# Kernel optimization log

Hardware: AMD Instinct MI355X
Metric: run time of the kernel (lower is better)

Reference implementation:

```python
import jax, jax.numpy as jnp
import numpy as np

WIRES = 4
NUM_LAYERS = 2


def setup_inputs() -> dict:
    key = jax.random.key(0)
    k1, k2 = jax.random.split(key)
    x = jax.random.uniform(k1, (8192, 1, 28, 28), dtype=jnp.float32)
    params = jax.random.normal(k2, (NUM_LAYERS, WIRES), dtype=jnp.float32)
    return {"x": x, "params": params}


def _apply_ry(state, theta, wire):
    # state: (B, P, 2,2,2,2) real (RY/CNOT circuit keeps amplitudes real)
    s = jnp.moveaxis(state, 2 + wire, -1)
    a, b = s[..., 0], s[..., 1]
    theta = jnp.asarray(theta)
    theta = theta.reshape(theta.shape + (1,) * (a.ndim - theta.ndim))
    c, sn = jnp.cos(theta / 2), jnp.sin(theta / 2)
    s = jnp.stack([c * a - sn * b, sn * a + c * b], axis=-1)
    return jnp.moveaxis(s, -1, 2 + wire)


def _cnot(state, ctrl, tgt):
    s = jnp.moveaxis(state, (2 + ctrl, 2 + tgt), (-2, -1))
    s = jnp.stack([s[..., 0, :], s[..., 1, ::-1]], axis=-2)
    return jnp.moveaxis(s, (-2, -1), (2 + ctrl, 2 + tgt))


def reference(x, params):
    B = x.shape[0]
    # 2x2 patches, row-major over (r, c); each flattened as [x00, x01, x10, x11]
    patches = x[:, 0].reshape(B, 14, 2, 14, 2).transpose(0, 1, 3, 2, 4).reshape(B, 196, 4)
    # |0000> for every (batch, patch)
    state = jnp.zeros((B, 196, 2, 2, 2, 2), dtype=x.dtype).at[:, :, 0, 0, 0, 0].set(1.0)
    # data-encoding RYs + entangling CNOT chain
    for w in range(WIRES):
        state = _apply_ry(state, patches[..., w], w)
    for w in range(WIRES - 1):
        state = _cnot(state, w, w + 1)
    # variational layers
    for layer in range(params.shape[0]):
        for w in range(WIRES):
            state = _apply_ry(state, params[layer, w], w)
        for w in range(WIRES - 1):
            state = _cnot(state, w, w + 1)
    # <Z_w> = P(bit_w = 0) - P(bit_w = 1)
    probs = state * state
    zs = []
    for w in range(WIRES):
        p = jnp.moveaxis(probs, 2 + w, 2)
        zs.append(p[:, :, 0].sum(axis=(2, 3, 4)) - p[:, :, 1].sum(axis=(2, 3, 4)))
    z = jnp.stack(zs, axis=-1)  # (B, 196, 4): 4 expvals per patch, patch-major
    return z.reshape(B, 196 * WIRES)
```

## Files before the change

kernel.cpp:

```cpp
#include <hip/hip_runtime.h>


typedef float f32x2 __attribute__((ext_vector_type(2)));

#define REV 0.07957747155f

__device__ __forceinline__ float fsin(float rev) {
    float o; asm("v_sin_f32 %0, %1" : "=v"(o) : "v"(rev)); return o;
}
__device__ __forceinline__ float fcos(float rev) {
    float o; asm("v_cos_f32 %0, %1" : "=v"(o) : "v"(rev)); return o;
}
__device__ __forceinline__ f32x2 pk_fma(f32x2 a, f32x2 b, f32x2 c) {
    return __builtin_elementwise_fma(a, b, c);
}
__device__ __forceinline__ f32x2 splat(float v) { return (f32x2){v, v}; }

__device__ __forceinline__ void pk_sincos_half(f32x2 x, f32x2& s, f32x2& c) {
    f32x2 t = x * 0.5f;
    f32x2 u = t * t;
    f32x2 ps = pk_fma(u, splat(8.3333333e-3f), splat(-0.16666667f));
    s = t * pk_fma(u, ps, splat(1.0f));
    f32x2 pc = pk_fma(u, splat(-1.3888889e-3f), splat(4.1666667e-2f));
    pc = pk_fma(u, pc, splat(-0.5f));
    c = pk_fma(u, pc, splat(1.0f));
}

template <int W>
__device__ __forceinline__ void apply_ry_t(f32x2 st[16], f32x2 tb, f32x2 ntb) {
    constexpr int S = 8 >> W;
#pragma unroll
    for (int i = 0; i < 16; ++i) {
        if ((i & S) == 0) {
            f32x2 a = st[i], b = st[i | S];
            st[i]     = pk_fma(ntb, b, a);
            st[i | S] = pk_fma(tb, a, b);
        }
    }
}

template <int C, int T>
__device__ __forceinline__ void cnot(f32x2 st[16]) {
    constexpr int CS = 8 >> C, TS = 8 >> T;
#pragma unroll
    for (int i = 0; i < 16; ++i) {
        if ((i & CS) != 0 && (i & TS) == 0) {
            f32x2 t = st[i];
            st[i] = st[i | TS];
            st[i | TS] = t;
        }
    }
}

__device__ __forceinline__ void circuit_pair(float4 top, float4 bot,
                                             const f32x2 tv[8], const f32x2 ntv[8],
                                             f32x2 scale, float4& o0, float4& o1) {
    f32x2 sw[4], cw[4];
    pk_sincos_half((f32x2){top.x, top.z}, sw[0], cw[0]);
    pk_sincos_half((f32x2){top.y, top.w}, sw[1], cw[1]);
    pk_sincos_half((f32x2){bot.x, bot.z}, sw[2], cw[2]);
    pk_sincos_half((f32x2){bot.y, bot.w}, sw[3], cw[3]);

    f32x2 st[16];
    {
        f32x2 r00 = cw[0] * cw[1], r01 = cw[0] * sw[1];
        f32x2 r10 = sw[0] * cw[1], r11 = sw[0] * sw[1];
        f32x2 q00 = cw[2] * cw[3], q01 = cw[2] * sw[3];
        f32x2 q10 = sw[2] * cw[3], q11 = sw[2] * sw[3];
        st[0]  = r00 * q00; st[1]  = r00 * q01; st[2]  = r00 * q10; st[3]  = r00 * q11;
        st[4]  = r01 * q00; st[5]  = r01 * q01; st[6]  = r01 * q10; st[7]  = r01 * q11;
        st[8]  = r10 * q00; st[9]  = r10 * q01; st[10] = r10 * q10; st[11] = r10 * q11;
        st[12] = r11 * q00; st[13] = r11 * q01; st[14] = r11 * q10; st[15] = r11 * q11;
    }

    cnot<0, 1>(st); cnot<1, 2>(st); cnot<2, 3>(st);

    apply_ry_t<0>(st, tv[0], ntv[0]);
    apply_ry_t<1>(st, tv[1], ntv[1]);
    apply_ry_t<2>(st, tv[2], ntv[2]);
    apply_ry_t<3>(st, tv[3], ntv[3]);
    cnot<0, 1>(st); cnot<1, 2>(st); cnot<2, 3>(st);
    apply_ry_t<0>(st, tv[4], ntv[4]);
    apply_ry_t<1>(st, tv[5], ntv[5]);
    apply_ry_t<2>(st, tv[6], ntv[6]);
    apply_ry_t<3>(st, tv[7], ntv[7]);
    cnot<0, 1>(st); cnot<1, 2>(st); cnot<2, 3>(st);

#pragma unroll
    for (int k = 0; k < 16; ++k) st[k] = st[k] * st[k];

    f32x2 a0 = st[0] + st[1],   d0 = st[0] - st[1];
    f32x2 a1 = st[2] + st[3],   d1 = st[2] - st[3];
    f32x2 a2 = st[4] + st[5],   d2 = st[4] - st[5];
    f32x2 a3 = st[6] + st[7],   d3 = st[6] - st[7];
    f32x2 a4 = st[8] + st[9],   d4 = st[8] - st[9];
    f32x2 a5 = st[10] + st[11], d5 = st[10] - st[11];
    f32x2 a6 = st[12] + st[13], d6 = st[12] - st[13];
    f32x2 a7 = st[14] + st[15], d7 = st[14] - st[15];
    f32x2 z3 = ((d0 + d1) + (d2 + d3)) + ((d4 + d5) + (d6 + d7));
    f32x2 b0 = a0 + a1, b1 = a2 + a3, b2 = a4 + a5, b3 = a6 + a7;
    f32x2 z2 = (a0 - a1) + (a2 - a3) + (a4 - a5) + (a6 - a7);
    f32x2 z1 = (b0 - b1) + (b2 - b3);
    f32x2 z0 = (b0 + b1) - (b2 + b3);
    z0 *= scale; z1 *= scale; z2 *= scale; z3 *= scale;

    o0 = make_float4(z0.x, z1.x, z2.x, z3.x);
    o1 = make_float4(z0.y, z1.y, z2.y, z3.y);
}

template <int K>
__global__ __launch_bounds__(256) void quanv_kernel(
    const float* __restrict__ x,
    const float* __restrict__ params,
    float* __restrict__ out,
    int chunkPairs,
    int chunkElems)
{
    int i = blockIdx.x * 256 + threadIdx.x;
    if (i >= chunkPairs) return;

    int b  = i / 98;
    int q  = i - b * 98;
    int r  = q / 7;
    int cp = q - r * 7;

    const float* base = x + (size_t)b * 784 + r * 56 + cp * 4;
    float4 L[2 * K];
#pragma unroll
    for (int k = 0; k < K; ++k) {
        const float* p = base + (size_t)k * chunkElems;
        L[2 * k]     = *reinterpret_cast<const float4*>(p);
        L[2 * k + 1] = *reinterpret_cast<const float4*>(p + 28);
    }

    f32x2 tv[8], ntv[8];
    float P = 1.0f;
#pragma unroll
    for (int k = 0; k < 8; ++k) {
        float rev = params[k] * REV;
        float s = fsin(rev), c = fcos(rev);
        float t = s * __builtin_amdgcn_rcpf(c);
        tv[k] = splat(t);
        ntv[k] = splat(-t);
        P *= c * c;
    }
    f32x2 scale = splat(P);

    float* obase = out + ((size_t)b * 196 + r * 14 + cp * 2) * 4;
#pragma unroll
    for (int k = 0; k < K; ++k) {
        float4 o0, o1;
        circuit_pair(L[2 * k], L[2 * k + 1], tv, ntv, scale, o0, o1);
        float* op = obase + (size_t)k * chunkElems;
        reinterpret_cast<float4*>(op)[0] = o0;
        reinterpret_cast<float4*>(op)[1] = o1;
    }
}

extern "C" void kernel_launch(void* const* d_in, const int* in_sizes, int n_in,
                              void* d_out, int out_size, void* d_ws, size_t ws_size,
                              hipStream_t stream) {
    const float* x      = (const float*)d_in[0];
    const float* params = (const float*)d_in[1];
    float* out = (float*)d_out;

    int B = in_sizes[0] / 784;

    if ((B % 4) == 0) {
        int chunkPairs = (B / 4) * 98;
        int chunkElems = (B / 4) * 784;
        int grid = (chunkPairs + 255) / 256;
        quanv_kernel<4><<<grid, 256, 0, stream>>>(x, params, out, chunkPairs, chunkElems);
    } else {
        int chunkPairs = B * 98;
        int grid = (chunkPairs + 255) / 256;
        quanv_kernel<1><<<grid, 256, 0, stream>>>(x, params, out, chunkPairs, B * 784);
    }
}
```

Before: 18.01 us.

## Use one patch pair per thread with nontemporal stores and no bounds guard

Replaces the four-chunks-per-thread scheme with one patch pair per thread over the whole batch, launching four times as many threads. The hope is that more parallelism and a minimum-occupancy launch bound hide memory latency better than batching loads inside a thread. It also adds nontemporal output stores and a guard-free template variant for when the grid divides evenly. The cost is that per-thread parameter trig setup is now repeated for every pair rather than shared across four, and there is less memory-level parallelism within each thread.

```diff
diff --git a/kernel.cpp b/kernel.cpp
--- a/kernel.cpp
+++ b/kernel.cpp
@@ -2,6 +2,7 @@
 
 
 typedef float f32x2 __attribute__((ext_vector_type(2)));
+typedef float f32x4 __attribute__((ext_vector_type(4)));
 
 #define REV 0.07957747155f
 
@@ -52,9 +53,38 @@
     }
 }
 
-__device__ __forceinline__ void circuit_pair(float4 top, float4 bot,
-                                             const f32x2 tv[8], const f32x2 ntv[8],
-                                             f32x2 scale, float4& o0, float4& o1) {
+template <bool GUARD>
+__global__ __launch_bounds__(256, 6) void quanv_kernel(
+    const float* __restrict__ x,
+    const float* __restrict__ params,
+    float* __restrict__ out,
+    int totalPairs)
+{
+    int i = blockIdx.x * 256 + threadIdx.x;
+    if (GUARD && i >= totalPairs) return;
+
+    int b  = i / 98;
+    int q  = i - b * 98;
+    int r  = q / 7;
+    int cp = q - r * 7;
+
+    const float* base = x + (size_t)b * 784 + r * 56 + cp * 4;
+    f32x4 top = *reinterpret_cast<const f32x4*>(base);
+    f32x4 bot = *reinterpret_cast<const f32x4*>(base + 28);
+
+    f32x2 tv[8], ntv[8];
+    float P = 1.0f;
+#pragma unroll
+    for (int k = 0; k < 8; ++k) {
+        float rev = params[k] * REV;
+        float s = fsin(rev), c = fcos(rev);
+        float t = s * __builtin_amdgcn_rcpf(c);
+        tv[k] = splat(t);
+        ntv[k] = splat(-t);
+        P *= c * c;
+    }
+    f32x2 scale = splat(P);
+
     f32x2 sw[4], cw[4];
     pk_sincos_half((f32x2){top.x, top.z}, sw[0], cw[0]);
     pk_sincos_half((f32x2){top.y, top.w}, sw[1], cw[1]);
@@ -104,57 +134,11 @@
     f32x2 z0 = (b0 + b1) - (b2 + b3);
     z0 *= scale; z1 *= scale; z2 *= scale; z3 *= scale;
 
-    o0 = make_float4(z0.x, z1.x, z2.x, z3.x);
-    o1 = make_float4(z0.y, z1.y, z2.y, z3.y);
-}
-
-template <int K>
-__global__ __launch_bounds__(256) void quanv_kernel(
-    const float* __restrict__ x,
-    const float* __restrict__ params,
-    float* __restrict__ out,
-    int chunkPairs,
-    int chunkElems)
-{
-    int i = blockIdx.x * 256 + threadIdx.x;
-    if (i >= chunkPairs) return;
-
-    int b  = i / 98;
-    int q  = i - b * 98;
-    int r  = q / 7;
-    int cp = q - r * 7;
-
-    const float* base = x + (size_t)b * 784 + r * 56 + cp * 4;
-    float4 L[2 * K];
-#pragma unroll
-    for (int k = 0; k < K; ++k) {
-        const float* p = base + (size_t)k * chunkElems;
-        L[2 * k]     = *reinterpret_cast<const float4*>(p);
-        L[2 * k + 1] = *reinterpret_cast<const float4*>(p + 28);
-    }
-
-    f32x2 tv[8], ntv[8];
-    float P = 1.0f;
-#pragma unroll
-    for (int k = 0; k < 8; ++k) {
-        float rev = params[k] * REV;
-        float s = fsin(rev), c = fcos(rev);
-        float t = s * __builtin_amdgcn_rcpf(c);
-        tv[k] = splat(t);
-        ntv[k] = splat(-t);
-        P *= c * c;
-    }
-    f32x2 scale = splat(P);
-
-    float* obase = out + ((size_t)b * 196 + r * 14 + cp * 2) * 4;
-#pragma unroll
-    for (int k = 0; k < K; ++k) {
-        float4 o0, o1;
-        circuit_pair(L[2 * k], L[2 * k + 1], tv, ntv, scale, o0, o1);
-        float* op = obase + (size_t)k * chunkElems;
-        reinterpret_cast<float4*>(op)[0] = o0;
-        reinterpret_cast<float4*>(op)[1] = o1;
-    }
+    float* op = out + ((size_t)b * 196 + r * 14 + cp * 2) * 4;
+    __builtin_nontemporal_store((f32x4){z0.x, z1.x, z2.x, z3.x},
+                                reinterpret_cast<f32x4*>(op));
+    __builtin_nontemporal_store((f32x4){z0.y, z1.y, z2.y, z3.y},
+                                reinterpret_cast<f32x4*>(op) + 1);
 }
 
 extern "C" void kernel_launch(void* const* d_in, const int* in_sizes, int n_in,
@@ -165,15 +149,11 @@
     float* out = (float*)d_out;
 
     int B = in_sizes[0] / 784;
+    int totalPairs = B * 98;
 
-    if ((B % 4) == 0) {
-        int chunkPairs = (B / 4) * 98;
-        int chunkElems = (B / 4) * 784;
-        int grid = (chunkPairs + 255) / 256;
-        quanv_kernel<4><<<grid, 256, 0, stream>>>(x, params, out, chunkPairs, chunkElems);
+    if ((totalPairs & 255) == 0) {
+        quanv_kernel<false><<<totalPairs / 256, 256, 0, stream>>>(x, params, out, totalPairs);
     } else {
-        int chunkPairs = B * 98;
-        int grid = (chunkPairs + 255) / 256;
-        quanv_kernel<1><<<grid, 256, 0, stream>>>(x, params, out, chunkPairs, B * 784);
+        quanv_kernel<true><<<(totalPairs + 255) / 256, 256, 0, stream>>>(x, params, out, totalPairs);
     }
 }
```

Result: faster. 16.20 us (-10.0%).
